# Performance work log

Hardware: AMD Instinct MI355X
Metric: run time of the kernel (lower is better)

The kernel has to match this reference:

```python
import jax, jax.numpy as jnp
import numpy as np

# Problem dims (match init_kwargs)
N, D, H, W = 32, 64, 56, 56      # Xshape
F, P = 128, 4                    # n_filters, number_of_points
KH = 3                           # h_filter == w_filter
PAD = KH // 2                    # padw
ALPHA = 0.1                      # threshold sharpness for sigmoid approximation


def setup_inputs() -> dict:
    key = jax.random.key(0)
    k1, k2, k3 = jax.random.split(key, 3)
    return {
        "input": jax.random.normal(k1, (N, D, H, W), dtype=jnp.float32),
        # integer kernel coordinates in [0, KH): (filter, point, [ky, kx])
        "kernels": jax.random.randint(k2, (F, P, 2), 0, KH, dtype=jnp.int32),
        # channel projection indices in [0, D): (filter, point)
        "projection_map": jax.random.randint(k3, (F, P), 0, D, dtype=jnp.int32),
    }


def _lbp_forward(x, kernels, projection_map):
    # Pad spatially by PAD (zero padding), as the CUDA kernel pads input.
    xp = jnp.pad(x, ((0, 0), (0, 0), (PAD, PAD), (PAD, PAD)))  # [N, D, H+2P, W+2P]

    # Per (filter, point): gather the HxW window at integer offset (ky, kx)
    # from channel c of the padded input. vmap of dynamic_slice -> one fused gather.
    def sample(c, ky, kx):
        return jax.lax.dynamic_slice(xp, (0, c, ky, kx), (N, 1, H, W))[:, 0]  # [N,H,W]

    samp = jax.vmap(jax.vmap(sample))(
        projection_map, kernels[..., 0], kernels[..., 1]
    )  # [F, P, N, H, W]
    samp = jnp.transpose(samp, (2, 0, 1, 3, 4))  # [N, F, P, H, W]

    # Center pixel (same channel as the sampled point).
    center = xp[:, :, PAD:PAD + H, PAD:PAD + W]       # [N, D, H, W]
    cen = center[:, projection_map]                    # [N, F, P, H, W]

    # Output0: per-point sampled difference; threshold approximated by a
    # steep sigmoid (scale 1/ALPHA) so the op is differentiable, then pool
    # the P bits into a binary code with weights 2^p.
    diff = samp - cen                                  # [N, F, P, H, W]
    bits = jax.nn.sigmoid(diff / ALPHA)
    weights = jnp.asarray(2.0 ** np.arange(P), dtype=jnp.float32)  # [P]
    return jnp.einsum('nfphw,p->nfhw', bits, weights)  # [N, F, H, W]


def reference(input, kernels, projection_map):
    return _lbp_forward(input, kernels, projection_map)
```

## Files before the change

### kernel.cpp

```cpp
#include <hip/hip_runtime.h>


#define NN 32
#define DD 64
#define HH 56
#define WW 56
#define FF 128
#define PP 4

#define ROWS 7
#define TR   (ROWS + 2)
#define TC   64
#define COL0 4
#define CHS  (TR * TC)
#define TILE_FLOATS (DD * CHS)
#define NTHREADS 1024
#define NWAVES 16
#define FITER (FF / NWAVES)
#define ITEMS (DD * TR * 14)

__global__ __launch_bounds__(NTHREADS, 4) void lbp_kernel(
    const float* __restrict__ x,
    const int*   __restrict__ kern,
    const int*   __restrict__ proj,
    float*       __restrict__ out)
{
    __shared__ float tile[TILE_FLOATS];

    const int tid = threadIdx.x;
    const int n   = blockIdx.y;
    const int h0  = blockIdx.x * ROWS;

    const float* xn = x + (size_t)n * (DD * HH * WW);

    float4 rv[8];
    int    lo[8];
#pragma unroll
    for (int it = 0; it < 8; ++it) {
        const int item = tid + it * NTHREADS;
        rv[it] = make_float4(0.f, 0.f, 0.f, 0.f);
        lo[it] = -1;
        if (item < ITEMS) {
            const int ch  = item / (TR * 14);
            const int rem = item - ch * (TR * 14);
            const int tr  = rem / 14;
            const int v   = rem - tr * 14;
            lo[it] = ch * CHS + tr * TC + COL0 + 4 * v;
            const int h = h0 + tr - 1;
            if ((unsigned)h < (unsigned)HH)
                rv[it] = *(const float4*)(xn + ch * (HH * WW) + h * WW + 4 * v);
        }
    }

    for (int i = tid; i < DD * TR * 2; i += NTHREADS) {
        const int ch   = i / (TR * 2);
        const int rr   = (i >> 1) % TR;
        const int side = i & 1;
        tile[ch * CHS + rr * TC + 3 + side * 57] = 0.f;
    }

#pragma unroll
    for (int it = 0; it < 8; ++it)
        if (lo[it] >= 0) *(float4*)(tile + lo[it]) = rv[it];
    __syncthreads();

    const int wid  = __builtin_amdgcn_readfirstlane(tid >> 6);
    const int lane = tid & 63;
    const int w    = lane < WW ? lane : WW - 1;
    const bool act = lane < WW;
    const int cb   = TC + COL0 + w;

    int f = wid;
    int4 pj = *(const int4*)(proj + f * PP);
    int4 ka = *(const int4*)(kern + f * (PP * 2));
    int4 kb = *(const int4*)(kern + f * (PP * 2) + 4);

#pragma unroll
    for (int k = 0; k < FITER; ++k) {
        const int fn = f + NWAVES;
        int4 pjn, kan, kbn;
        if (fn < FF) {
            pjn = *(const int4*)(proj + fn * PP);
            kan = *(const int4*)(kern + fn * (PP * 2));
            kbn = *(const int4*)(kern + fn * (PP * 2) + 4);
        }
        const int cc[4]  = {pj.x, pj.y, pj.z, pj.w};
        const int kyv[4] = {ka.x, ka.z, kb.x, kb.z};
        const int kxv[4] = {ka.y, ka.w, kb.y, kb.w};

        float cv[PP][ROWS], nv[PP][ROWS];
#pragma unroll
        for (int p = 0; p < PP; ++p) {
            const int pc = cc[p] * CHS + cb;
            const int pn = pc + (kyv[p] - 1) * TC + (kxv[p] - 1);
#pragma unroll
            for (int r = 0; r < ROWS; ++r) {
                cv[p][r] = tile[pc + r * TC];
                nv[p][r] = tile[pn + r * TC];
            }
        }

        float acc[ROWS];
#pragma unroll
        for (int r = 0; r < ROWS; ++r) acc[r] = 7.5f;
#pragma unroll
        for (int p = 0; p < PP; ++p) {
            const float wt = (float)(1 << p);
#pragma unroll
            for (int r = 0; r < ROWS; ++r) {
                const float d  = nv[p][r] - cv[p][r];
                const float ad = __builtin_fabsf(d);
                const float u0 = fmaf(2.5f,     ad, -0.0078f);
                const float u1 = fmaf(1.49146f, ad,  0.08455f);
                const float u2 = fmaf(0.45177f, ad,  0.30774f);
                const float um = fminf(fminf(fminf(u0, u1), u2), 0.49140f);
                acc[r] = fmaf(wt, __builtin_copysignf(um, d), acc[r]);
            }
        }

        if (act) {
            float* op = out + ((size_t)n * FF + f) * (HH * WW)
                            + (size_t)h0 * WW + w;
#pragma unroll
            for (int r = 0; r < ROWS; ++r) op[r * WW] = acc[r];
        }
        f = fn; pj = pjn; ka = kan; kb = kbn;
    }
}

extern "C" void kernel_launch(void* const* d_in, const int* in_sizes, int n_in,
                              void* d_out, int out_size, void* d_ws, size_t ws_size,
                              hipStream_t stream) {
    const float* x    = (const float*)d_in[0];
    const int*   kern = (const int*)d_in[1];
    const int*   proj = (const int*)d_in[2];
    float*       out  = (float*)d_out;

    dim3 grid(HH / ROWS, NN);
    dim3 block(NTHREADS);
    lbp_kernel<<<grid, block, 0, stream>>>(x, kern, proj, out);
}
```

Before: 26.63 us.

## Drop LDS tile staging; read neighbors directly from global with filter-group split grid

Removes the shared-memory staging of all 64 channels per row strip and has each lane load center and neighbor pixels straight from global memory, handling zero padding with lane and strip masks. The grid is split four ways over filter groups, with 512-thread blocks each covering 32 filters, for more blocks and higher occupancy. This avoids loading every channel into LDS when only the projected channels are used, and drops the block barrier. In exchange, overlapping neighbor reads go through L1/L2 and become partly scattered global loads, and each input strip is fetched by four blocks.

```diff
diff --git a/kernel.cpp b/kernel.cpp
--- a/kernel.cpp
+++ b/kernel.cpp
@@ -9,77 +9,45 @@
 #define PP 4
 
 #define ROWS 7
-#define TR   (ROWS + 2)
-#define TC   64
-#define COL0 4
-#define CHS  (TR * TC)
-#define TILE_FLOATS (DD * CHS)
-#define NTHREADS 1024
-#define NWAVES 16
-#define FITER (FF / NWAVES)
-#define ITEMS (DD * TR * 14)
+#define NSTRIP 8
+#define NTHREADS 512
+#define FPB 32
+#define FPW 4
 
-__global__ __launch_bounds__(NTHREADS, 4) void lbp_kernel(
+__global__ __launch_bounds__(NTHREADS, 8) void lbp_kernel(
     const float* __restrict__ x,
     const int*   __restrict__ kern,
     const int*   __restrict__ proj,
     float*       __restrict__ out)
 {
-    __shared__ float tile[TILE_FLOATS];
+    const int tid   = threadIdx.x;
+    const int n     = blockIdx.x;
+    const int strip = blockIdx.y >> 2;
+    const int fg    = blockIdx.y & 3;
+    const int h0    = strip * ROWS;
 
-    const int tid = threadIdx.x;
-    const int n   = blockIdx.y;
-    const int h0  = blockIdx.x * ROWS;
+    const int wave = __builtin_amdgcn_readfirstlane(tid >> 6);
+    const int lane = tid & 63;
+    const int w    = lane < WW ? lane : WW - 1;
+    const bool act = lane < WW;
+    const bool e0  = (lane == 0);
+    const bool e1  = (lane >= WW - 1);
+
+    const int w0 = (w > 0) ? (w - 1) : 0;
+    const int w2 = (w < WW - 1) ? (w + 1) : (WW - 1);
 
     const float* xn = x + (size_t)n * (DD * HH * WW);
 
-    float4 rv[8];
-    int    lo[8];
-#pragma unroll
-    for (int it = 0; it < 8; ++it) {
-        const int item = tid + it * NTHREADS;
-        rv[it] = make_float4(0.f, 0.f, 0.f, 0.f);
-        lo[it] = -1;
-        if (item < ITEMS) {
-            const int ch  = item / (TR * 14);
-            const int rem = item - ch * (TR * 14);
-            const int tr  = rem / 14;
-            const int v   = rem - tr * 14;
-            lo[it] = ch * CHS + tr * TC + COL0 + 4 * v;
-            const int h = h0 + tr - 1;
-            if ((unsigned)h < (unsigned)HH)
-                rv[it] = *(const float4*)(xn + ch * (HH * WW) + h * WW + 4 * v);
-        }
-    }
-
-    for (int i = tid; i < DD * TR * 2; i += NTHREADS) {
-        const int ch   = i / (TR * 2);
-        const int rr   = (i >> 1) % TR;
-        const int side = i & 1;
-        tile[ch * CHS + rr * TC + 3 + side * 57] = 0.f;
-    }
-
-#pragma unroll
-    for (int it = 0; it < 8; ++it)
-        if (lo[it] >= 0) *(float4*)(tile + lo[it]) = rv[it];
-    __syncthreads();
-
-    const int wid  = __builtin_amdgcn_readfirstlane(tid >> 6);
-    const int lane = tid & 63;
-    const int w    = lane < WW ? lane : WW - 1;
-    const bool act = lane < WW;
-    const int cb   = TC + COL0 + w;
-
-    int f = wid;
+    int f = fg * FPB + wave;
     int4 pj = *(const int4*)(proj + f * PP);
     int4 ka = *(const int4*)(kern + f * (PP * 2));
     int4 kb = *(const int4*)(kern + f * (PP * 2) + 4);
 
 #pragma unroll
-    for (int k = 0; k < FITER; ++k) {
-        const int fn = f + NWAVES;
+    for (int k = 0; k < FPW; ++k) {
+        const int fn = f + 8;
         int4 pjn, kan, kbn;
-        if (fn < FF) {
+        if (k + 1 < FPW) {
             pjn = *(const int4*)(proj + fn * PP);
             kan = *(const int4*)(kern + fn * (PP * 2));
             kbn = *(const int4*)(kern + fn * (PP * 2) + 4);
@@ -88,27 +56,43 @@
         const int kyv[4] = {ka.x, ka.z, kb.x, kb.z};
         const int kxv[4] = {ka.y, ka.w, kb.y, kb.w};
 
-        float cv[PP][ROWS], nv[PP][ROWS];
-#pragma unroll
-        for (int p = 0; p < PP; ++p) {
-            const int pc = cc[p] * CHS + cb;
-            const int pn = pc + (kyv[p] - 1) * TC + (kxv[p] - 1);
-#pragma unroll
-            for (int r = 0; r < ROWS; ++r) {
-                cv[p][r] = tile[pc + r * TC];
-                nv[p][r] = tile[pn + r * TC];
-            }
-        }
-
         float acc[ROWS];
 #pragma unroll
         for (int r = 0; r < ROWS; ++r) acc[r] = 7.5f;
+
 #pragma unroll
         for (int p = 0; p < PP; ++p) {
+            const int ky = kyv[p];
+            const int kx = kxv[p];
+            const float* cb = xn + cc[p] * (HH * WW) + h0 * WW;
+            const float* nbase = cb + (ky - 1) * WW;
+            const int wn = (kx == 0) ? w0 : ((kx == 2) ? w2 : w);
+
+            float cv[ROWS], nv[ROWS];
+#pragma unroll
+            for (int r = 0; r < ROWS; ++r)
+                cv[r] = cb[r * WW + w];
+            const bool topOOB = (strip == 0)          && (ky == 0);
+            const bool botOOB = (strip == NSTRIP - 1) && (ky == 2);
+#pragma unroll
+            for (int r = 0; r < ROWS; ++r) {
+                if ((r == 0 && topOOB) || (r == ROWS - 1 && botOOB))
+                    nv[r] = 0.f;
+                else
+                    nv[r] = nbase[r * WW + wn];
+            }
+            if (kx == 0) {
+#pragma unroll
+                for (int r = 0; r < ROWS; ++r) nv[r] = e0 ? 0.f : nv[r];
+            } else if (kx == 2) {
+#pragma unroll
+                for (int r = 0; r < ROWS; ++r) nv[r] = e1 ? 0.f : nv[r];
+            }
+
             const float wt = (float)(1 << p);
 #pragma unroll
             for (int r = 0; r < ROWS; ++r) {
-                const float d  = nv[p][r] - cv[p][r];
+                const float d  = nv[r] - cv[r];
                 const float ad = __builtin_fabsf(d);
                 const float u0 = fmaf(2.5f,     ad, -0.0078f);
                 const float u1 = fmaf(1.49146f, ad,  0.08455f);
@@ -136,7 +120,7 @@
     const int*   proj = (const int*)d_in[2];
     float*       out  = (float*)d_out;
 
-    dim3 grid(HH / ROWS, NN);
+    dim3 grid(NN, NSTRIP * 4);
     dim3 block(NTHREADS);
     lbp_kernel<<<grid, block, 0, stream>>>(x, kern, proj, out);
 }
```

Result: slower. 37.30 us (+40.0%).

## Transpose LDS tile to column-major rows with swizzle; fetch halo rows from global

Applied to the files above, without the earlier changes.

The shared-memory tile is rearranged so each column holds its 7 rows contiguously in an 8-float slot, XOR-swizzled to avoid bank conflicts. Each point can then be read with two 128-bit LDS loads instead of many scalar loads. Halo rows above and below the strip are no longer staged; they are read directly from global memory per point, and the grid is reordered to batch-major. The change cuts LDS footprint and LDS instruction count, at the cost of branchy per-point global halo loads and scattered scalar writes into the tile.

```diff
diff --git a/kernel.cpp b/kernel.cpp
--- a/kernel.cpp
+++ b/kernel.cpp
@@ -9,15 +9,17 @@
 #define PP 4
 
 #define ROWS 7
-#define TR   (ROWS + 2)
-#define TC   64
-#define COL0 4
-#define CHS  (TR * TC)
-#define TILE_FLOATS (DD * CHS)
+#define NSTRIP 8
 #define NTHREADS 1024
 #define NWAVES 16
 #define FITER (FF / NWAVES)
-#define ITEMS (DD * TR * 14)
+#define NCOLP 58
+#define SLOT  8
+#define CHDW  (NCOLP * SLOT)
+#define TILE_DW (DD * CHDW)
+#define NITEMS (DD * ROWS * 14)
+
+__device__ __forceinline__ int swzb(int colp) { return ((colp >> 2) & 3) << 4; }
 
 __global__ __launch_bounds__(NTHREADS, 4) void lbp_kernel(
     const float* __restrict__ x,
@@ -25,50 +27,62 @@
     const int*   __restrict__ proj,
     float*       __restrict__ out)
 {
-    __shared__ float tile[TILE_FLOATS];
+    __shared__ float tile[TILE_DW];
+    char* tb = (char*)tile;
 
-    const int tid = threadIdx.x;
-    const int n   = blockIdx.y;
-    const int h0  = blockIdx.x * ROWS;
+    const int tid   = threadIdx.x;
+    const int n     = blockIdx.x;
+    const int strip = blockIdx.y;
+    const int h0    = strip * ROWS;
 
     const float* xn = x + (size_t)n * (DD * HH * WW);
 
-    float4 rv[8];
-    int    lo[8];
+    float4 rv[7];
 #pragma unroll
-    for (int it = 0; it < 8; ++it) {
+    for (int it = 0; it < 7; ++it) {
         const int item = tid + it * NTHREADS;
-        rv[it] = make_float4(0.f, 0.f, 0.f, 0.f);
-        lo[it] = -1;
-        if (item < ITEMS) {
-            const int ch  = item / (TR * 14);
-            const int rem = item - ch * (TR * 14);
-            const int tr  = rem / 14;
-            const int v   = rem - tr * 14;
-            lo[it] = ch * CHS + tr * TC + COL0 + 4 * v;
-            const int h = h0 + tr - 1;
-            if ((unsigned)h < (unsigned)HH)
-                rv[it] = *(const float4*)(xn + ch * (HH * WW) + h * WW + 4 * v);
+        if (item < NITEMS) {
+            const int ch  = item / (ROWS * 14);
+            const int rem = item - ch * (ROWS * 14);
+            const int r   = rem / 14;
+            const int g   = rem - r * 14;
+            rv[it] = *(const float4*)(xn + ch * (HH * WW) + (h0 + r) * WW + 4 * g);
         }
     }
 
-    for (int i = tid; i < DD * TR * 2; i += NTHREADS) {
-        const int ch   = i / (TR * 2);
-        const int rr   = (i >> 1) % TR;
-        const int side = i & 1;
-        tile[ch * CHS + rr * TC + 3 + side * 57] = 0.f;
+    if (tid < 256) {
+        const int ch   = tid >> 2;
+        const int colp = ((tid >> 1) & 1) ? 57 : 0;
+        const int half = tid & 1;
+        const int b = (((ch * NCOLP + colp) * SLOT) * 4 + half * 16) ^ swzb(colp);
+        *(float4*)(tb + b) = make_float4(0.f, 0.f, 0.f, 0.f);
     }
 
 #pragma unroll
-    for (int it = 0; it < 8; ++it)
-        if (lo[it] >= 0) *(float4*)(tile + lo[it]) = rv[it];
+    for (int it = 0; it < 7; ++it) {
+        const int item = tid + it * NTHREADS;
+        if (item < NITEMS) {
+            const int ch  = item / (ROWS * 14);
+            const int rem = item - ch * (ROWS * 14);
+            const int r   = rem / 14;
+            const int g   = rem - r * 14;
+            const float4 v = rv[it];
+            const int base = ch * CHDW + r;
+#pragma unroll
+            for (int j = 0; j < 4; ++j) {
+                const int colp = 1 + 4 * g + j;
+                const float e = (j == 0) ? v.x : (j == 1) ? v.y : (j == 2) ? v.z : v.w;
+                const int b = ((base + colp * SLOT) * 4) ^ swzb(colp);
+                *(float*)(tb + b) = e;
+            }
+        }
+    }
     __syncthreads();
 
     const int wid  = __builtin_amdgcn_readfirstlane(tid >> 6);
     const int lane = tid & 63;
-    const int w    = lane < WW ? lane : WW - 1;
+    const int w    = (lane < WW) ? lane : (lane - WW);
     const bool act = lane < WW;
-    const int cb   = TC + COL0 + w;
 
     int f = wid;
     int4 pj = *(const int4*)(proj + f * PP);
@@ -88,27 +102,63 @@
         const int kyv[4] = {ka.x, ka.z, kb.x, kb.z};
         const int kxv[4] = {ka.y, ka.w, kb.y, kb.w};
 
-        float cv[PP][ROWS], nv[PP][ROWS];
-#pragma unroll
-        for (int p = 0; p < PP; ++p) {
-            const int pc = cc[p] * CHS + cb;
-            const int pn = pc + (kyv[p] - 1) * TC + (kxv[p] - 1);
-#pragma unroll
-            for (int r = 0; r < ROWS; ++r) {
-                cv[p][r] = tile[pc + r * TC];
-                nv[p][r] = tile[pn + r * TC];
-            }
-        }
-
         float acc[ROWS];
 #pragma unroll
         for (int r = 0; r < ROWS; ++r) acc[r] = 7.5f;
+
 #pragma unroll
         for (int p = 0; p < PP; ++p) {
+            const int c  = cc[p];
+            const int ky = kyv[p];
+            const int kx = kxv[p];
+
+            float gt = 0.f, gb = 0.f;
+            if (ky == 0) {
+                if (strip > 0) {
+                    int wn = w + kx - 1; wn = (wn < 0) ? 0 : (wn > 55 ? 55 : wn);
+                    gt = xn[c * (HH * WW) + (h0 - 1) * WW + wn];
+                    if (kx == 0) gt = (lane == 0) ? 0.f : gt;
+                    if (kx == 2) gt = (lane == 55) ? 0.f : gt;
+                }
+            } else if (ky == 2) {
+                if (strip < NSTRIP - 1) {
+                    int wn = w + kx - 1; wn = (wn < 0) ? 0 : (wn > 55 ? 55 : wn);
+                    gb = xn[c * (HH * WW) + (h0 + ROWS) * WW + wn];
+                    if (kx == 0) gb = (lane == 0) ? 0.f : gb;
+                    if (kx == 2) gb = (lane == 55) ? 0.f : gb;
+                }
+            }
+
+            const int cp  = w + 1;
+            const int cb0 = ((c * CHDW + cp * SLOT) * 4);
+            const float4 c0 = *(const float4*)(tb + ((cb0)      ^ swzb(cp)));
+            const float4 c1 = *(const float4*)(tb + ((cb0 + 16) ^ swzb(cp)));
+
+            float4 n0 = c0, n1 = c1;
+            if (kx != 1) {
+                const int cq  = w + kx;
+                const int nb0 = ((c * CHDW + cq * SLOT) * 4);
+                n0 = *(const float4*)(tb + ((nb0)      ^ swzb(cq)));
+                n1 = *(const float4*)(tb + ((nb0 + 16) ^ swzb(cq)));
+            }
+
+            const float C[ROWS] = {c0.x, c0.y, c0.z, c0.w, c1.x, c1.y, c1.z};
+            float Nv[ROWS];
+            if (ky == 0) {
+                Nv[0] = gt;   Nv[1] = n0.x; Nv[2] = n0.y; Nv[3] = n0.z;
+                Nv[4] = n0.w; Nv[5] = n1.x; Nv[6] = n1.y;
+            } else if (ky == 1) {
+                Nv[0] = n0.x; Nv[1] = n0.y; Nv[2] = n0.z; Nv[3] = n0.w;
+                Nv[4] = n1.x; Nv[5] = n1.y; Nv[6] = n1.z;
+            } else {
+                Nv[0] = n0.y; Nv[1] = n0.z; Nv[2] = n0.w; Nv[3] = n1.x;
+                Nv[4] = n1.y; Nv[5] = n1.z; Nv[6] = gb;
+            }
+
             const float wt = (float)(1 << p);
 #pragma unroll
             for (int r = 0; r < ROWS; ++r) {
-                const float d  = nv[p][r] - cv[p][r];
+                const float d  = Nv[r] - C[r];
                 const float ad = __builtin_fabsf(d);
                 const float u0 = fmaf(2.5f,     ad, -0.0078f);
                 const float u1 = fmaf(1.49146f, ad,  0.08455f);
@@ -136,7 +186,7 @@
     const int*   proj = (const int*)d_in[2];
     float*       out  = (float*)d_out;
 
-    dim3 grid(HH / ROWS, NN);
+    dim3 grid(NN, NSTRIP);
     dim3 block(NTHREADS);
     lbp_kernel<<<grid, block, 0, stream>>>(x, kern, proj, out);
 }
```

New measurement: 30.51 us. 1.15x slower.
